# Kernel tuning notes

Measured on AMD Instinct MI355X. Metric: run time of the kernel, lower is better.

## Reference

```python
import jax, jax.numpy as jnp
import numpy as np

B, S, D, H = 2, 2048, 1024, 16
HD = D // H  # head_dim = 64


def setup_inputs() -> dict:
    key = jax.random.key(0)
    ks = jax.random.split(key, 12)
    scale = 1.0 / np.sqrt(D)
    inp = {
        "query": jax.random.normal(ks[0], (B, S, D), jnp.float32),
        "key": jax.random.normal(ks[1], (B, S, D), jnp.float32),
        "value": jax.random.normal(ks[2], (B, S, D), jnp.float32),
        # causal mask, True = masked out; shape [B, q_len, k_len]
        "mask": jnp.broadcast_to(
            jnp.triu(jnp.ones((S, S), jnp.bool_), k=1), (B, S, S)
        ),
        "Wq": jax.random.normal(ks[3], (D, D), jnp.float32) * scale,
        "bq": jnp.zeros((D,), jnp.float32),
        "Wk": jax.random.normal(ks[4], (D, D), jnp.float32) * scale,
        "bk": jnp.zeros((D,), jnp.float32),
        "Wv": jax.random.normal(ks[5], (D, D), jnp.float32) * scale,
        "bv": jnp.zeros((D,), jnp.float32),
        "Wo": jax.random.normal(ks[6], (D, D), jnp.float32) * scale,
        "bo": jnp.zeros((D,), jnp.float32),
    }
    return inp


def _split_heads(x):
    b, s, _ = x.shape
    return x.reshape(b, s, H, HD).transpose(0, 2, 1, 3)  # [B,H,S,HD]


def reference(query, key, value, mask, Wq, bq, Wk, bk, Wv, bv, Wo, bo):
    # Linear layers use torch convention: y = x @ W.T + b, W is [out, in]
    q = _split_heads(query @ Wq.T + bq)
    k = _split_heads(key @ Wk.T + bk)
    v = _split_heads(value @ Wv.T + bv)
    scores = jnp.einsum("bhqd,bhkd->bhqk", q, k) / jnp.sqrt(jnp.float32(HD))
    # normalized mask [B,1,q,k]; True means masked
    scores = jnp.where(mask[:, None, :, :], jnp.finfo(scores.dtype).min, scores)
    attn = jax.nn.softmax(scores, axis=-1)  # dropout is identity in eval
    ctx = jnp.einsum("bhqk,bhkd->bhqd", attn, v)
    merged = ctx.transpose(0, 2, 1, 3).reshape(query.shape[0], -1, D)
    out = merged @ Wo.T + bo
    return out
```

## Files before the change

kernel.cpp:

```cpp
#include <hip/hip_runtime.h>

#define B_ 2
#define S_ 2048
#define D_ 1024
#define H_ 16
#define HD_ 64
#define M_ (B_ * S_)

typedef __bf16 bf16x8 __attribute__((ext_vector_type(8)));
typedef float f32x4 __attribute__((ext_vector_type(4)));

__device__ inline unsigned short f2bf(float f) {
    unsigned int u = __builtin_bit_cast(unsigned int, f);
    u += 0x7fffu + ((u >> 16) & 1u);
    return (unsigned short)(u >> 16);
}

__device__ inline unsigned int cvt_pk_bf16(float lo, float hi) {
    unsigned int r;
    asm("v_cvt_pk_bf16_f32 %0, %1, %2" : "=v"(r) : "v"(lo), "v"(hi));
    return r;
}

__device__ inline float fexp2(float x) { return __builtin_amdgcn_exp2f(x); }

__device__ inline void barrier_fence() {
    asm volatile("" ::: "memory");
    __builtin_amdgcn_s_barrier();
    asm volatile("" ::: "memory");
}

__device__ inline void async_ld16(const unsigned short* g, unsigned short* l) {
    __builtin_amdgcn_global_load_lds(
        (const __attribute__((address_space(1))) unsigned int*)g,
        (__attribute__((address_space(3))) unsigned int*)l, 16, 0, 0);
}

__global__ __launch_bounds__(256) void cvt_all(
    const float* __restrict__ i0, const float* __restrict__ i1, const float* __restrict__ i2,
    const float* __restrict__ i3, const float* __restrict__ i4, const float* __restrict__ i5,
    const float* __restrict__ i6,
    unsigned short* __restrict__ o0, unsigned short* __restrict__ o1, unsigned short* __restrict__ o2,
    unsigned short* __restrict__ o3, unsigned short* __restrict__ o4, unsigned short* __restrict__ o5,
    unsigned short* __restrict__ o6, int nbig, int nsmall) {
    int z = blockIdx.y;
    const float* in = (z == 0) ? i0 : (z == 1) ? i1 : (z == 2) ? i2 : (z == 3) ? i3
                     : (z == 4) ? i4 : (z == 5) ? i5 : i6;
    unsigned short* out = (z == 0) ? o0 : (z == 1) ? o1 : (z == 2) ? o2 : (z == 3) ? o3
                         : (z == 4) ? o4 : (z == 5) ? o5 : o6;
    int n = (z < 3) ? nbig : nsmall;
    int i = (blockIdx.x * 256 + threadIdx.x) * 4;
    if (i >= n) return;
    float4 v = *(const float4*)(in + i);
    ushort4 o;
    o.x = f2bf(v.x); o.y = f2bf(v.y); o.z = f2bf(v.z); o.w = f2bf(v.w);
    *(ushort4*)(out + i) = o;
}

__device__ inline void gemm_compute(const unsigned short* __restrict__ A,
                                    const unsigned short* __restrict__ W,
                                    int K, int m0, int n0,
                                    unsigned short* As0, unsigned short* As1,
                                    unsigned short* Bs0, unsigned short* Bs1,
                                    f32x4 acc[4][4]) {
    const int t = threadIdx.x;
    const int lane = t & 63, wave = t >> 6;
    const int ml = lane & 15, quad = lane >> 4;
    const int wr = (wave >> 1) * 64, wc = (wave & 1) * 64;
    const int srow = lane >> 2;
    const int schunk = (lane & 3) ^ ((lane >> 4) & 3);

    const f32x4 zero = {0.f, 0.f, 0.f, 0.f};
    for (int i = 0; i < 4; i++)
        for (int j = 0; j < 4; j++) acc[i][j] = zero;

    const int niter = K >> 5;

    auto issue = [&](int kt, unsigned short* As, unsigned short* Bs) {
        int k0 = kt << 5;
        for (int i = 0; i < 2; i++) {
            int r = wave * 32 + i * 16;
            async_ld16(A + (size_t)(m0 + r + srow) * K + k0 + schunk * 8, As + r * 32);
            async_ld16(W + (size_t)(n0 + r + srow) * K + k0 + schunk * 8, Bs + r * 32);
        }
    };

    issue(0, As0, Bs0);
    issue(1, As1, Bs1);
    asm volatile("s_waitcnt vmcnt(4)" ::: "memory");
    barrier_fence();

    for (int kt = 0; kt < niter; kt++) {
        unsigned short* As = (kt & 1) ? As1 : As0;
        unsigned short* Bs = (kt & 1) ? Bs1 : Bs0;

        bf16x8 af[4], bfr[4];
        for (int i = 0; i < 4; i++)
            af[i] = *(const bf16x8*)(As + (wr + i * 16 + ml) * 32 + ((quad ^ (ml >> 2)) << 3));
        for (int j = 0; j < 4; j++)
            bfr[j] = *(const bf16x8*)(Bs + (wc + j * 16 + ml) * 32 + ((quad ^ (ml >> 2)) << 3));
        for (int i = 0; i < 4; i++)
            for (int j = 0; j < 4; j++)
                acc[i][j] = __builtin_amdgcn_mfma_f32_16x16x32_bf16(af[i], bfr[j], acc[i][j], 0, 0, 0);

        barrier_fence();
        if (kt + 2 < niter) {
            issue(kt + 2, As, Bs);
            asm volatile("s_waitcnt vmcnt(4)" ::: "memory");
        } else {
            asm volatile("s_waitcnt vmcnt(0)" ::: "memory");
        }
        barrier_fence();
    }
}

__global__ __launch_bounds__(256) void gemm_qkv(
    const unsigned short* __restrict__ xq, const unsigned short* __restrict__ xk,
    const unsigned short* __restrict__ xv,
    const unsigned short* __restrict__ wq, const unsigned short* __restrict__ wk,
    const unsigned short* __restrict__ wv,
    const float* __restrict__ bq, const float* __restrict__ bk, const float* __restrict__ bv,
    unsigned short* __restrict__ oq, unsigned short* __restrict__ ok,
    unsigned short* __restrict__ ov) {
    extern __shared__ __align__(16) unsigned short smem[];
    unsigned short* As0 = smem;
    unsigned short* As1 = smem + 4096;
    unsigned short* Bs0 = smem + 8192;
    unsigned short* Bs1 = smem + 12288;

    int f = blockIdx.x + (blockIdx.y << 3) + (blockIdx.z << 8);
    int l = (f & 7) * 96 + (f >> 3);
    int bx = l & 7, by = (l >> 3) & 31, z = l >> 8;

    const unsigned short *A, *W;
    const float* bias;
    unsigned short* out;
    if (z == 0) { A = xq; W = wq; bias = bq; out = oq; }
    else if (z == 1) { A = xk; W = wk; bias = bk; out = ok; }
    else { A = xv; W = wv; bias = bv; out = ov; }

    int m0 = by * 128, n0 = bx * 128;
    f32x4 acc[4][4];
    gemm_compute(A, W, D_, m0, n0, As0, As1, Bs0, Bs1, acc);

    const int t = threadIdx.x, lane = t & 63, wave = t >> 6;
    const int ml = lane & 15, quad = lane >> 4;
    const int wr = (wave >> 1) * 64, wc = (wave & 1) * 64;

    unsigned short* Cs = smem;
    const float sc = (z == 0) ? 0.1803368801111204f : 1.0f;
    for (int i = 0; i < 4; i++)
        for (int j = 0; j < 4; j++) {
            int col = wc + j * 16 + ml;
            float bb = bias[n0 + col];
            for (int rg = 0; rg < 4; rg++) {
                int row = wr + i * 16 + quad * 4 + rg;
                unsigned short v = f2bf((acc[i][j][rg] + bb) * sc);
                if (z < 2) Cs[row * 136 + col] = v;
                else       Cs[col * 136 + row] = v;
            }
        }
    __syncthreads();

    const int r = t >> 1, hf = t & 1;
    if (z < 2) {
        unsigned short* dst = out + (size_t)(m0 + r) * D_ + n0 + hf * 64;
        const unsigned short* src = Cs + r * 136 + hf * 64;
        for (int i = 0; i < 8; i++)
            *(uint4*)(dst + i * 8) = *(const uint4*)(src + i * 8);
    } else {
        int n = n0 + r, h = n >> 6, d = n & 63;
        int b = m0 >> 11, s0 = m0 & 2047;
        unsigned short* dst = ov + ((size_t)((b * H_ + h) * 64 + d)) * S_ + s0 + hf * 64;
        const unsigned short* src = Cs + r * 136 + hf * 64;
        for (int i = 0; i < 8; i++)
            *(uint4*)(dst + i * 8) = *(const uint4*)(src + i * 8);
    }
}

__global__ __launch_bounds__(256) void gemm_out(const unsigned short* __restrict__ A,
                                                const unsigned short* __restrict__ W,
                                                const float* __restrict__ bias,
                                                float* __restrict__ out) {
    __shared__ unsigned short As0[128 * 32], As1[128 * 32], Bs0[128 * 32], Bs1[128 * 32];

    int f = blockIdx.x + (blockIdx.y << 3);
    int l = (f & 7) * 32 + (f >> 3);
    int bx = l & 7, by = l >> 3;

    int m0 = by * 128, n0 = bx * 128;
    f32x4 acc[4][4];
    gemm_compute(A, W, D_, m0, n0, As0, As1, Bs0, Bs1, acc);

    const int t = threadIdx.x, lane = t & 63, wave = t >> 6;
    const int ml = lane & 15, quad = lane >> 4;
    const int wr = (wave >> 1) * 64, wc = (wave & 1) * 64;
    for (int i = 0; i < 4; i++)
        for (int j = 0; j < 4; j++) {
            int n = n0 + wc + j * 16 + ml;
            float bb = bias[n];
            for (int rg = 0; rg < 4; rg++) {
                int m = m0 + wr + i * 16 + quad * 4 + rg;
                out[(size_t)m * D_ + n] = acc[i][j][rg] + bb;
            }
        }
}

__global__ __launch_bounds__(256) void attn_kernel(const unsigned short* __restrict__ qm,
                                                   const unsigned short* __restrict__ km,
                                                   const unsigned short* __restrict__ vt,
                                                   unsigned short* __restrict__ ctx) {
    __shared__ unsigned short Ks[2][128 * 64];
    __shared__ unsigned short Vs[64 * 128];

    const int qb = 31 - (blockIdx.x >> 5);
    const int bh = blockIdx.x & 31;
    const int b = bh >> 4, h = bh & 15;
    const size_t vbase = (size_t)bh * S_ * 64;
    const int t = threadIdx.x, lane = t & 63, wave = t >> 6;
    const int ml = lane & 15, quad = lane >> 4;
    const int lrow = lane >> 3;
    const int gchunk = (lane & 7) ^ lrow;
    const int vrow = lane >> 4;
    const int q0 = qb * 64;

    bf16x8 qf[2];
    {
        int qrow = q0 + wave * 16 + ml;
        const unsigned short* qp = qm + (size_t)(b * S_ + qrow) * D_ + h * 64;
        qf[0] = *(const bf16x8*)(qp + quad * 8);
        qf[1] = *(const bf16x8*)(qp + 32 + quad * 8);
    }

    const f32x4 zero = {0.f, 0.f, 0.f, 0.f};
    f32x4 acc[4];
    for (int j = 0; j < 4; j++) acc[j] = zero;
    float m_i = -INFINITY, l_i = 0.f;

    const int ntiles = (qb + 2) >> 1;

    auto issue_K = [&](int kt, int bb) {
        for (int i = 0; i < 4; i++) {
            int r = wave * 32 + i * 8;
            async_ld16(km + (size_t)(b * S_ + kt * 128 + r + lrow) * D_ + h * 64 + gchunk * 8,
                       Ks[bb] + r * 64);
        }
    };
    auto issue_V = [&](int kt) {
        for (int i = 0; i < 4; i++) {
            int dd = wave * 16 + i * 4;
            int d = dd + vrow;
            async_ld16(vt + vbase + (size_t)d * S_ + kt * 128 + (((lane & 15) ^ (d & 15)) << 3),
                       Vs + dd * 128);
        }
    };

    issue_K(0, 0);
    issue_V(0);
    issue_K(1, 1);
    asm volatile("s_waitcnt vmcnt(8)" ::: "memory");
    barrier_fence();

    for (int kt = 0; kt < ntiles; kt++) {
        const int buf = kt & 1;

        f32x4 sacc[8];
        for (int n = 0; n < 8; n++) sacc[n] = zero;
        __builtin_amdgcn_s_setprio(1);
        for (int n = 0; n < 8; n++)
            for (int kk = 0; kk < 2; kk++) {
                bf16x8 kf = *(const bf16x8*)(Ks[buf] + (n * 16 + ml) * 64 +
                                             (((kk * 4 + quad) ^ (ml & 7)) << 3));
                sacc[n] = __builtin_amdgcn_mfma_f32_16x16x32_bf16(kf, qf[kk], sacc[n], 0, 0, 0);
            }
        __builtin_amdgcn_s_setprio(0);

        const bool last = (kt == ntiles - 1);
        const int qidx = q0 + wave * 16 + ml;
        if (last) {
            for (int n = 0; n < 8; n++)
                for (int rg = 0; rg < 4; rg++) {
                    int kidx = kt * 128 + n * 16 + quad * 4 + rg;
                    if (kidx > qidx) sacc[n][rg] = -3.0e38f;
                }
        }

        float mx = sacc[0][0];
        for (int n = 0; n < 8; n++)
            for (int rg = 0; rg < 4; rg++) mx = fmaxf(mx, sacc[n][rg]);
        mx = fmaxf(mx, __shfl_xor(mx, 16));
        mx = fmaxf(mx, __shfl_xor(mx, 32));
        float mc = fmaxf(m_i, mx);
        float al = fexp2(m_i - mc);
        m_i = mc;
        float rs = 0.f;
        for (int n = 0; n < 8; n++)
            for (int rg = 0; rg < 4; rg++) {
                float p = fexp2(sacc[n][rg] - mc);
                sacc[n][rg] = p;
                rs += p;
            }
        rs += __shfl_xor(rs, 16);
        rs += __shfl_xor(rs, 32);
        l_i = l_i * al + rs;

        float alT[4];
        for (int rg = 0; rg < 4; rg++) alT[rg] = __shfl(al, quad * 4 + rg);
        for (int j = 0; j < 4; j++)
            for (int rg = 0; rg < 4; rg++) acc[j][rg] *= alT[rg];

        asm volatile("s_waitcnt vmcnt(0)" ::: "memory");
        barrier_fence();

        if (kt + 2 < ntiles) issue_K(kt + 2, buf);

        __builtin_amdgcn_s_setprio(1);
        for (int n2 = 0; n2 < 4; n2++) {
            union { bf16x8 v; unsigned int w[4]; } pk;
            pk.w[0] = cvt_pk_bf16(sacc[2 * n2][0], sacc[2 * n2][1]);
            pk.w[1] = cvt_pk_bf16(sacc[2 * n2][2], sacc[2 * n2][3]);
            pk.w[2] = cvt_pk_bf16(sacc[2 * n2 + 1][0], sacc[2 * n2 + 1][1]);
            pk.w[3] = cvt_pk_bf16(sacc[2 * n2 + 1][2], sacc[2 * n2 + 1][3]);
            const int c0 = 4 * n2 + (quad >> 1);
            const int qo = (quad & 1) << 2;
            for (int j = 0; j < 4; j++) {
                int row = j * 16 + ml;
                union { bf16x8 v; uint2 d2[2]; } vv;
                vv.d2[0] = *(const uint2*)(Vs + row * 128 + (((c0 ^ (row & 15)) << 3) + qo));
                vv.d2[1] = *(const uint2*)(Vs + row * 128 + ((((c0 + 2) ^ (row & 15)) << 3) + qo));
                acc[j] = __builtin_amdgcn_mfma_f32_16x16x32_bf16(pk.v, vv.v, acc[j], 0, 0, 0);
            }
        }
        __builtin_amdgcn_s_setprio(0);

        barrier_fence();
        if (kt + 1 < ntiles) issue_V(kt + 1);
    }

    float inv[4];
    for (int rg = 0; rg < 4; rg++) inv[rg] = __builtin_amdgcn_rcpf(__shfl(l_i, quad * 4 + rg));
    for (int j = 0; j < 4; j++) {
        int d = j * 16 + ml;
        for (int rg = 0; rg < 4; rg++) {
            int srow = q0 + wave * 16 + quad * 4 + rg;
            ctx[((size_t)(b * S_ + srow)) * D_ + h * 64 + d] = f2bf(acc[j][rg] * inv[rg]);
        }
    }
}

extern "C" void kernel_launch(void* const* d_in, const int* in_sizes, int n_in,
                              void* d_out, int out_size, void* d_ws, size_t ws_size,
                              hipStream_t stream) {
    const float* query = (const float*)d_in[0];
    const float* key_ = (const float*)d_in[1];
    const float* value = (const float*)d_in[2];
    const float* Wq = (const float*)d_in[4];
    const float* bq = (const float*)d_in[5];
    const float* Wk = (const float*)d_in[6];
    const float* bk = (const float*)d_in[7];
    const float* Wv = (const float*)d_in[8];
    const float* bv = (const float*)d_in[9];
    const float* Wo = (const float*)d_in[10];
    const float* bo = (const float*)d_in[11];
    float* out = (float*)d_out;

    const size_t XE = (size_t)M_ * D_;
    const size_t WE = (size_t)D_ * D_;
    char* ws = (char*)d_ws;
    unsigned short* xq = (unsigned short*)ws; ws += XE * 2;
    unsigned short* xk = (unsigned short*)ws; ws += XE * 2;
    unsigned short* xv = (unsigned short*)ws; ws += XE * 2;
    unsigned short* wqb = (unsigned short*)ws; ws += WE * 2;
    unsigned short* wkb = (unsigned short*)ws; ws += WE * 2;
    unsigned short* wvb = (unsigned short*)ws; ws += WE * 2;
    unsigned short* wob = (unsigned short*)ws; ws += WE * 2;
    unsigned short* qmb = (unsigned short*)ws; ws += XE * 2;
    unsigned short* kmb = (unsigned short*)ws; ws += XE * 2;
    unsigned short* vt = (unsigned short*)ws; ws += XE * 2;
    unsigned short* ctx = (unsigned short*)ws; ws += XE * 2;

    cvt_all<<<dim3(XE / 1024, 7), 256, 0, stream>>>(
        query, key_, value, Wq, Wk, Wv, Wo,
        xq, xk, xv, wqb, wkb, wvb, wob, (int)XE, (int)WE);

    gemm_qkv<<<dim3(D_ / 128, M_ / 128, 3), 256, 34816, stream>>>(
        xq, xk, xv, wqb, wkb, wvb, bq, bk, bv, qmb, kmb, vt);

    attn_kernel<<<dim3(1024), 256, 0, stream>>>(qmb, kmb, vt, ctx);

    gemm_out<<<dim3(D_ / 128, M_ / 128), 256, 0, stream>>>(ctx, wob, bo, out);
}
```

Measured before the change: 243.0 us.

## Single-buffer K tile, lazy softmax rescale, interleave query-block order, tree reductions

The K shared buffer drops from double to single, which lowers LDS use per block and may allow more resident blocks. The price is that the K prefetch is issued only one tile ahead, after the S computation. Online-softmax rescaling of the accumulator is skipped unless the new row max exceeds the running max by more than 8 (lazy rescale). Query blocks are interleaved heavy/light to balance causal work across the grid. Max and sum reductions are rewritten as trees to shorten dependency chains.

```diff
diff --git a/kernel.cpp b/kernel.cpp
--- a/kernel.cpp
+++ b/kernel.cpp
@@ -210,10 +210,11 @@
                                                    const unsigned short* __restrict__ km,
                                                    const unsigned short* __restrict__ vt,
                                                    unsigned short* __restrict__ ctx) {
-    __shared__ unsigned short Ks[2][128 * 64];
+    __shared__ unsigned short Ks[128 * 64];
     __shared__ unsigned short Vs[64 * 128];
 
-    const int qb = 31 - (blockIdx.x >> 5);
+    const int g = blockIdx.x >> 5;
+    const int qb = (g & 1) ? (g >> 1) : (31 - (g >> 1));
     const int bh = blockIdx.x & 31;
     const int b = bh >> 4, h = bh & 15;
     const size_t vbase = (size_t)bh * S_ * 64;
@@ -239,11 +240,11 @@
 
     const int ntiles = (qb + 2) >> 1;
 
-    auto issue_K = [&](int kt, int bb) {
+    auto issue_K = [&](int kt) {
         for (int i = 0; i < 4; i++) {
             int r = wave * 32 + i * 8;
             async_ld16(km + (size_t)(b * S_ + kt * 128 + r + lrow) * D_ + h * 64 + gchunk * 8,
-                       Ks[bb] + r * 64);
+                       Ks + r * 64);
         }
     };
     auto issue_V = [&](int kt) {
@@ -255,21 +256,18 @@
         }
     };
 
-    issue_K(0, 0);
+    issue_K(0);
     issue_V(0);
-    issue_K(1, 1);
-    asm volatile("s_waitcnt vmcnt(8)" ::: "memory");
+    asm volatile("s_waitcnt vmcnt(0)" ::: "memory");
     barrier_fence();
 
     for (int kt = 0; kt < ntiles; kt++) {
-        const int buf = kt & 1;
-
         f32x4 sacc[8];
         for (int n = 0; n < 8; n++) sacc[n] = zero;
         __builtin_amdgcn_s_setprio(1);
         for (int n = 0; n < 8; n++)
             for (int kk = 0; kk < 2; kk++) {
-                bf16x8 kf = *(const bf16x8*)(Ks[buf] + (n * 16 + ml) * 64 +
+                bf16x8 kf = *(const bf16x8*)(Ks + (n * 16 + ml) * 64 +
                                              (((kk * 4 + quad) ^ (ml & 7)) << 3));
                 sacc[n] = __builtin_amdgcn_mfma_f32_16x16x32_bf16(kf, qf[kk], sacc[n], 0, 0, 0);
             }
@@ -285,34 +283,46 @@
                 }
         }
 
-        float mx = sacc[0][0];
-        for (int n = 0; n < 8; n++)
-            for (int rg = 0; rg < 4; rg++) mx = fmaxf(mx, sacc[n][rg]);
+        float m01 = fmaxf(fmaxf(sacc[0][0], sacc[0][1]), fmaxf(sacc[0][2], sacc[0][3]));
+        float m1 = fmaxf(fmaxf(sacc[1][0], sacc[1][1]), fmaxf(sacc[1][2], sacc[1][3]));
+        float m2 = fmaxf(fmaxf(sacc[2][0], sacc[2][1]), fmaxf(sacc[2][2], sacc[2][3]));
+        float m3 = fmaxf(fmaxf(sacc[3][0], sacc[3][1]), fmaxf(sacc[3][2], sacc[3][3]));
+        float m4 = fmaxf(fmaxf(sacc[4][0], sacc[4][1]), fmaxf(sacc[4][2], sacc[4][3]));
+        float m5 = fmaxf(fmaxf(sacc[5][0], sacc[5][1]), fmaxf(sacc[5][2], sacc[5][3]));
+        float m6 = fmaxf(fmaxf(sacc[6][0], sacc[6][1]), fmaxf(sacc[6][2], sacc[6][3]));
+        float m7 = fmaxf(fmaxf(sacc[7][0], sacc[7][1]), fmaxf(sacc[7][2], sacc[7][3]));
+        float mx = fmaxf(fmaxf(fmaxf(m01, m1), fmaxf(m2, m3)),
+                         fmaxf(fmaxf(m4, m5), fmaxf(m6, m7)));
         mx = fmaxf(mx, __shfl_xor(mx, 16));
         mx = fmaxf(mx, __shfl_xor(mx, 32));
-        float mc = fmaxf(m_i, mx);
-        float al = fexp2(m_i - mc);
-        m_i = mc;
-        float rs = 0.f;
+        if (!__all(mx <= m_i + 8.0f)) {
+            float mc = fmaxf(m_i, mx);
+            float al = fexp2(m_i - mc);
+            m_i = mc;
+            float alT[4];
+            for (int rg = 0; rg < 4; rg++) alT[rg] = __shfl(al, quad * 4 + rg);
+            for (int j = 0; j < 4; j++)
+                for (int rg = 0; rg < 4; rg++) acc[j][rg] *= alT[rg];
+            l_i *= al;
+        }
         for (int n = 0; n < 8; n++)
-            for (int rg = 0; rg < 4; rg++) {
-                float p = fexp2(sacc[n][rg] - mc);
-                sacc[n][rg] = p;
-                rs += p;
-            }
+            for (int rg = 0; rg < 4; rg++) sacc[n][rg] = fexp2(sacc[n][rg] - m_i);
+        float s0 = (sacc[0][0] + sacc[0][1]) + (sacc[0][2] + sacc[0][3]);
+        float s1 = (sacc[1][0] + sacc[1][1]) + (sacc[1][2] + sacc[1][3]);
+        float s2 = (sacc[2][0] + sacc[2][1]) + (sacc[2][2] + sacc[2][3]);
+        float s3 = (sacc[3][0] + sacc[3][1]) + (sacc[3][2] + sacc[3][3]);
+        float s4 = (sacc[4][0] + sacc[4][1]) + (sacc[4][2] + sacc[4][3]);
+        float s5 = (sacc[5][0] + sacc[5][1]) + (sacc[5][2] + sacc[5][3]);
+        float s6 = (sacc[6][0] + sacc[6][1]) + (sacc[6][2] + sacc[6][3]);
+        float s7 = (sacc[7][0] + sacc[7][1]) + (sacc[7][2] + sacc[7][3]);
+        float rs = ((s0 + s1) + (s2 + s3)) + ((s4 + s5) + (s6 + s7));
         rs += __shfl_xor(rs, 16);
         rs += __shfl_xor(rs, 32);
-        l_i = l_i * al + rs;
-
-        float alT[4];
-        for (int rg = 0; rg < 4; rg++) alT[rg] = __shfl(al, quad * 4 + rg);
-        for (int j = 0; j < 4; j++)
-            for (int rg = 0; rg < 4; rg++) acc[j][rg] *= alT[rg];
+        l_i += rs;
 
         asm volatile("s_waitcnt vmcnt(0)" ::: "memory");
         barrier_fence();
-
-        if (kt + 2 < ntiles) issue_K(kt + 2, buf);
+        if (kt + 1 < ntiles) issue_K(kt + 1);
 
         __builtin_amdgcn_s_setprio(1);
         for (int n2 = 0; n2 < 4; n2++) {
@@ -333,8 +343,11 @@
         }
         __builtin_amdgcn_s_setprio(0);
 
-        barrier_fence();
-        if (kt + 1 < ntiles) issue_V(kt + 1);
+        if (kt + 1 < ntiles) {
+            asm volatile("s_waitcnt vmcnt(0)" ::: "memory");
+            barrier_fence();
+            issue_V(kt + 1);
+        }
     }
 
     float inv[4];
```

Result: no change. 240.1 us (-1.2%).

## Process two 64-row query sub-blocks per attention block with lazy rescaling

Applied to the files above, without the earlier changes.

Each attention block now handles 128 query rows as two 64-row halves that share every K/V tile loaded into shared memory, which halves the grid and the K/V traffic per query. V is double-buffered so the next K and V tiles are prefetched at the top of each iteration, and query blocks are ordered to interleave heavy and light causal work. The online-softmax rescale is skipped unless the running max grows by more than a threshold, and the row sums are reduced only once at the end. The trade-offs are higher register pressure (launch bounds now request 2 blocks per CU), more shared memory, and fewer blocks to spread across CUs.

```diff
diff --git a/kernel.cpp b/kernel.cpp
--- a/kernel.cpp
+++ b/kernel.cpp
@@ -206,14 +206,15 @@
         }
 }
 
-__global__ __launch_bounds__(256) void attn_kernel(const unsigned short* __restrict__ qm,
-                                                   const unsigned short* __restrict__ km,
-                                                   const unsigned short* __restrict__ vt,
-                                                   unsigned short* __restrict__ ctx) {
+__global__ __launch_bounds__(256, 2) void attn_kernel(const unsigned short* __restrict__ qm,
+                                                      const unsigned short* __restrict__ km,
+                                                      const unsigned short* __restrict__ vt,
+                                                      unsigned short* __restrict__ ctx) {
     __shared__ unsigned short Ks[2][128 * 64];
-    __shared__ unsigned short Vs[64 * 128];
-
-    const int qb = 31 - (blockIdx.x >> 5);
+    __shared__ unsigned short Vs[2][64 * 128];
+
+    const int g = blockIdx.x >> 5;
+    const int ip = (g < 8) ? (15 - g) : (g - 8);
     const int bh = blockIdx.x & 31;
     const int b = bh >> 4, h = bh & 15;
     const size_t vbase = (size_t)bh * S_ * 64;
@@ -222,22 +223,19 @@
     const int lrow = lane >> 3;
     const int gchunk = (lane & 7) ^ lrow;
     const int vrow = lane >> 4;
-    const int q0 = qb * 64;
-
-    bf16x8 qf[2];
+    const int q0 = ip * 128;
+    const int nt = ip + 1;
+
+    bf16x8 qfA[2], qfB[2];
     {
         int qrow = q0 + wave * 16 + ml;
         const unsigned short* qp = qm + (size_t)(b * S_ + qrow) * D_ + h * 64;
-        qf[0] = *(const bf16x8*)(qp + quad * 8);
-        qf[1] = *(const bf16x8*)(qp + 32 + quad * 8);
-    }
-
-    const f32x4 zero = {0.f, 0.f, 0.f, 0.f};
-    f32x4 acc[4];
-    for (int j = 0; j < 4; j++) acc[j] = zero;
-    float m_i = -INFINITY, l_i = 0.f;
-
-    const int ntiles = (qb + 2) >> 1;
+        qfA[0] = *(const bf16x8*)(qp + quad * 8);
+        qfA[1] = *(const bf16x8*)(qp + 32 + quad * 8);
+        const unsigned short* qp2 = qp + (size_t)64 * D_;
+        qfB[0] = *(const bf16x8*)(qp2 + quad * 8);
+        qfB[1] = *(const bf16x8*)(qp2 + 32 + quad * 8);
+    }
 
     auto issue_K = [&](int kt, int bb) {
         for (int i = 0; i < 4; i++) {
@@ -246,104 +244,156 @@
                        Ks[bb] + r * 64);
         }
     };
-    auto issue_V = [&](int kt) {
+    auto issue_V = [&](int kt, int bb) {
         for (int i = 0; i < 4; i++) {
             int dd = wave * 16 + i * 4;
             int d = dd + vrow;
             async_ld16(vt + vbase + (size_t)d * S_ + kt * 128 + (((lane & 15) ^ (d & 15)) << 3),
-                       Vs + dd * 128);
+                       Vs[bb] + dd * 128);
         }
     };
 
+    const f32x4 zero = {0.f, 0.f, 0.f, 0.f};
+    f32x4 accA[4], accB[4];
+    for (int j = 0; j < 4; j++) { accA[j] = zero; accB[j] = zero; }
+    float mA = -INFINITY, mB = -INFINITY, lpA = 0.f, lpB = 0.f;
+
     issue_K(0, 0);
-    issue_V(0);
-    issue_K(1, 1);
-    asm volatile("s_waitcnt vmcnt(8)" ::: "memory");
+    issue_V(0, 0);
+    asm volatile("s_waitcnt vmcnt(0)" ::: "memory");
     barrier_fence();
 
-    for (int kt = 0; kt < ntiles; kt++) {
+    for (int kt = 0; kt < nt; kt++) {
         const int buf = kt & 1;
-
-        f32x4 sacc[8];
-        for (int n = 0; n < 8; n++) sacc[n] = zero;
+        if (kt + 1 < nt) { issue_K(kt + 1, buf ^ 1); issue_V(kt + 1, buf ^ 1); }
+
+        f32x4 sA[8], sB[8];
+        for (int n = 0; n < 8; n++) { sA[n] = zero; sB[n] = zero; }
         __builtin_amdgcn_s_setprio(1);
         for (int n = 0; n < 8; n++)
             for (int kk = 0; kk < 2; kk++) {
                 bf16x8 kf = *(const bf16x8*)(Ks[buf] + (n * 16 + ml) * 64 +
                                              (((kk * 4 + quad) ^ (ml & 7)) << 3));
-                sacc[n] = __builtin_amdgcn_mfma_f32_16x16x32_bf16(kf, qf[kk], sacc[n], 0, 0, 0);
+                sA[n] = __builtin_amdgcn_mfma_f32_16x16x32_bf16(kf, qfA[kk], sA[n], 0, 0, 0);
+                sB[n] = __builtin_amdgcn_mfma_f32_16x16x32_bf16(kf, qfB[kk], sB[n], 0, 0, 0);
             }
         __builtin_amdgcn_s_setprio(0);
 
-        const bool last = (kt == ntiles - 1);
-        const int qidx = q0 + wave * 16 + ml;
-        if (last) {
+        const int qidxA = q0 + wave * 16 + ml;
+        const int qidxB = qidxA + 64;
+        if (kt == nt - 1) {
             for (int n = 0; n < 8; n++)
                 for (int rg = 0; rg < 4; rg++) {
                     int kidx = kt * 128 + n * 16 + quad * 4 + rg;
-                    if (kidx > qidx) sacc[n][rg] = -3.0e38f;
+                    if (kidx > qidxA) sA[n][rg] = -3.0e38f;
+                    if (kidx > qidxB) sB[n][rg] = -3.0e38f;
                 }
         }
 
-        float mx = sacc[0][0];
-        for (int n = 0; n < 8; n++)
-            for (int rg = 0; rg < 4; rg++) mx = fmaxf(mx, sacc[n][rg]);
-        mx = fmaxf(mx, __shfl_xor(mx, 16));
-        mx = fmaxf(mx, __shfl_xor(mx, 32));
-        float mc = fmaxf(m_i, mx);
-        float al = fexp2(m_i - mc);
-        m_i = mc;
-        float rs = 0.f;
+        float a0 = fmaxf(fmaxf(sA[0][0], sA[0][1]), fmaxf(sA[0][2], sA[0][3]));
+        float a1 = fmaxf(fmaxf(sA[1][0], sA[1][1]), fmaxf(sA[1][2], sA[1][3]));
+        float a2 = fmaxf(fmaxf(sA[2][0], sA[2][1]), fmaxf(sA[2][2], sA[2][3]));
+        float a3 = fmaxf(fmaxf(sA[3][0], sA[3][1]), fmaxf(sA[3][2], sA[3][3]));
+        float a4 = fmaxf(fmaxf(sA[4][0], sA[4][1]), fmaxf(sA[4][2], sA[4][3]));
+        float a5 = fmaxf(fmaxf(sA[5][0], sA[5][1]), fmaxf(sA[5][2], sA[5][3]));
+        float a6 = fmaxf(fmaxf(sA[6][0], sA[6][1]), fmaxf(sA[6][2], sA[6][3]));
+        float a7 = fmaxf(fmaxf(sA[7][0], sA[7][1]), fmaxf(sA[7][2], sA[7][3]));
+        float mxA = fmaxf(fmaxf(fmaxf(a0, a1), fmaxf(a2, a3)),
+                          fmaxf(fmaxf(a4, a5), fmaxf(a6, a7)));
+        float b0 = fmaxf(fmaxf(sB[0][0], sB[0][1]), fmaxf(sB[0][2], sB[0][3]));
+        float b1 = fmaxf(fmaxf(sB[1][0], sB[1][1]), fmaxf(sB[1][2], sB[1][3]));
+        float b2 = fmaxf(fmaxf(sB[2][0], sB[2][1]), fmaxf(sB[2][2], sB[2][3]));
+        float b3 = fmaxf(fmaxf(sB[3][0], sB[3][1]), fmaxf(sB[3][2], sB[3][3]));
+        float b4 = fmaxf(fmaxf(sB[4][0], sB[4][1]), fmaxf(sB[4][2], sB[4][3]));
+        float b5 = fmaxf(fmaxf(sB[5][0], sB[5][1]), fmaxf(sB[5][2], sB[5][3]));
+        float b6 = fmaxf(fmaxf(sB[6][0], sB[6][1]), fmaxf(sB[6][2], sB[6][3]));
+        float b7 = fmaxf(fmaxf(sB[7][0], sB[7][1]), fmaxf(sB[7][2], sB[7][3]));
+        float mxB = fmaxf(fmaxf(fmaxf(b0, b1), fmaxf(b2, b3)),
+                          fmaxf(fmaxf(b4, b5), fmaxf(b6, b7)));
+
+        if (!__all((mxA <= mA + 4.0f) & (mxB <= mB + 4.0f))) {
+            float mcA = fmaxf(mxA, __shfl_xor(mxA, 16));
+            mcA = fmaxf(mcA, __shfl_xor(mcA, 32));
+            mcA = fmaxf(mA, mcA);
+            float alA = fexp2(mA - mcA);
+            mA = mcA;
+            float mcB = fmaxf(mxB, __shfl_xor(mxB, 16));
+            mcB = fmaxf(mcB, __shfl_xor(mcB, 32));
+            mcB = fmaxf(mB, mcB);
+            float alB = fexp2(mB - mcB);
+            mB = mcB;
+            float aTA[4], aTB[4];
+            for (int rg = 0; rg < 4; rg++) {
+                aTA[rg] = __shfl(alA, quad * 4 + rg);
+                aTB[rg] = __shfl(alB, quad * 4 + rg);
+            }
+            for (int j = 0; j < 4; j++)
+                for (int rg = 0; rg < 4; rg++) {
+                    accA[j][rg] *= aTA[rg];
+                    accB[j][rg] *= aTB[rg];
+                }
+            lpA *= alA;
+            lpB *= alB;
+        }
+
         for (int n = 0; n < 8; n++)
             for (int rg = 0; rg < 4; rg++) {
-                float p = fexp2(sacc[n][rg] - mc);
-                sacc[n][rg] = p;
-                rs += p;
-            }
-        rs += __shfl_xor(rs, 16);
-        rs += __shfl_xor(rs, 32);
-        l_i = l_i * al + rs;
-
-        float alT[4];
-        for (int rg = 0; rg < 4; rg++) alT[rg] = __shfl(al, quad * 4 + rg);
-        for (int j = 0; j < 4; j++)
-            for (int rg = 0; rg < 4; rg++) acc[j][rg] *= alT[rg];
-
-        asm volatile("s_waitcnt vmcnt(0)" ::: "memory");
-        barrier_fence();
-
-        if (kt + 2 < ntiles) issue_K(kt + 2, buf);
+                sA[n][rg] = fexp2(sA[n][rg] - mA);
+                sB[n][rg] = fexp2(sB[n][rg] - mB);
+            }
+        {
+            float r0 = 0.f, r1 = 0.f;
+            for (int n = 0; n < 8; n++) {
+                r0 += (sA[n][0] + sA[n][1]) + (sA[n][2] + sA[n][3]);
+                r1 += (sB[n][0] + sB[n][1]) + (sB[n][2] + sB[n][3]);
+            }
+            lpA += r0;
+            lpB += r1;
+        }
 
         __builtin_amdgcn_s_setprio(1);
         for (int n2 = 0; n2 < 4; n2++) {
-            union { bf16x8 v; unsigned int w[4]; } pk;
-            pk.w[0] = cvt_pk_bf16(sacc[2 * n2][0], sacc[2 * n2][1]);
-            pk.w[1] = cvt_pk_bf16(sacc[2 * n2][2], sacc[2 * n2][3]);
-            pk.w[2] = cvt_pk_bf16(sacc[2 * n2 + 1][0], sacc[2 * n2 + 1][1]);
-            pk.w[3] = cvt_pk_bf16(sacc[2 * n2 + 1][2], sacc[2 * n2 + 1][3]);
+            union { bf16x8 v; unsigned int w[4]; } pkA, pkB;
+            pkA.w[0] = cvt_pk_bf16(sA[2 * n2][0], sA[2 * n2][1]);
+            pkA.w[1] = cvt_pk_bf16(sA[2 * n2][2], sA[2 * n2][3]);
+            pkA.w[2] = cvt_pk_bf16(sA[2 * n2 + 1][0], sA[2 * n2 + 1][1]);
+            pkA.w[3] = cvt_pk_bf16(sA[2 * n2 + 1][2], sA[2 * n2 + 1][3]);
+            pkB.w[0] = cvt_pk_bf16(sB[2 * n2][0], sB[2 * n2][1]);
+            pkB.w[1] = cvt_pk_bf16(sB[2 * n2][2], sB[2 * n2][3]);
+            pkB.w[2] = cvt_pk_bf16(sB[2 * n2 + 1][0], sB[2 * n2 + 1][1]);
+            pkB.w[3] = cvt_pk_bf16(sB[2 * n2 + 1][2], sB[2 * n2 + 1][3]);
             const int c0 = 4 * n2 + (quad >> 1);
             const int qo = (quad & 1) << 2;
             for (int j = 0; j < 4; j++) {
                 int row = j * 16 + ml;
                 union { bf16x8 v; uint2 d2[2]; } vv;
-                vv.d2[0] = *(const uint2*)(Vs + row * 128 + (((c0 ^ (row & 15)) << 3) + qo));
-                vv.d2[1] = *(const uint2*)(Vs + row * 128 + ((((c0 + 2) ^ (row & 15)) << 3) + qo));
-                acc[j] = __builtin_amdgcn_mfma_f32_16x16x32_bf16(pk.v, vv.v, acc[j], 0, 0, 0);
+                vv.d2[0] = *(const uint2*)(Vs[buf] + row * 128 + (((c0 ^ (row & 15)) << 3) + qo));
+                vv.d2[1] = *(const uint2*)(Vs[buf] + row * 128 + ((((c0 + 2) ^ (row & 15)) << 3) + qo));
+                accA[j] = __builtin_amdgcn_mfma_f32_16x16x32_bf16(pkA.v, vv.v, accA[j], 0, 0, 0);
+                accB[j] = __builtin_amdgcn_mfma_f32_16x16x32_bf16(pkB.v, vv.v, accB[j], 0, 0, 0);
             }
         }
         __builtin_amdgcn_s_setprio(0);
 
+        asm volatile("s_waitcnt vmcnt(0)" ::: "memory");
         barrier_fence();
-        if (kt + 1 < ntiles) issue_V(kt + 1);
-    }
-
-    float inv[4];
-    for (int rg = 0; rg < 4; rg++) inv[rg] = __builtin_amdgcn_rcpf(__shfl(l_i, quad * 4 + rg));
+    }
+
+    float lcA = lpA + __shfl_xor(lpA, 16);
+    lcA += __shfl_xor(lcA, 32);
+    float lcB = lpB + __shfl_xor(lpB, 16);
+    lcB += __shfl_xor(lcB, 32);
+    float invA[4], invB[4];
+    for (int rg = 0; rg < 4; rg++) {
+        invA[rg] = __builtin_amdgcn_rcpf(__shfl(lcA, quad * 4 + rg));
+        invB[rg] = __builtin_amdgcn_rcpf(__shfl(lcB, quad * 4 + rg));
+    }
     for (int j = 0; j < 4; j++) {
         int d = j * 16 + ml;
         for (int rg = 0; rg < 4; rg++) {
             int srow = q0 + wave * 16 + quad * 4 + rg;
-            ctx[((size_t)(b * S_ + srow)) * D_ + h * 64 + d] = f2bf(acc[j][rg] * inv[rg]);
+            ctx[((size_t)(b * S_ + srow)) * D_ + h * 64 + d] = f2bf(accA[j][rg] * invA[rg]);
+            ctx[((size_t)(b * S_ + srow + 64)) * D_ + h * 64 + d] = f2bf(accB[j][rg] * invB[rg]);
         }
     }
 }
@@ -386,7 +436,7 @@
     gemm_qkv<<<dim3(D_ / 128, M_ / 128, 3), 256, 34816, stream>>>(
         xq, xk, xv, wqb, wkb, wvb, bq, bk, bv, qmb, kmb, vt);
 
-    attn_kernel<<<dim3(1024), 256, 0, stream>>>(qmb, kmb, vt, ctx);
+    attn_kernel<<<dim3(512), 256, 0, stream>>>(qmb, kmb, vt, ctx);
 
     gemm_out<<<dim3(D_ / 128, M_ / 128), 256, 0, stream>>>(ctx, wob, bo, out);
 }
```

New measurement: 245.6 us. Within noise of the previous version (+1.1%).
